# Optimization experiments

Measured on AMD Instinct MI355X. Metric: run time of the kernel, lower is better.

## Reference

```python
import jax, jax.numpy as jnp
import numpy as np

B, D, C = 4096, 256, 64  # batch, dim_embed, n_conditions
EPS = 1e-10


def setup_inputs() -> dict:
    key = jax.random.key(0)
    k1, k2, k3, k4 = jax.random.split(key, 4)
    x = jax.random.normal(k1, (B, D), dtype=jnp.float32)          # embedded_x (embeddingnet = identity)
    W = jax.random.normal(k2, (C, D, D), dtype=jnp.float32) * 0.02  # per-condition Linear weights (out,in)
    b = jax.random.normal(k3, (C, D), dtype=jnp.float32) * 0.02     # per-condition Linear biases
    c = jax.random.randint(k4, (B,), 0, C)                         # condition index per sample
    return {"x": x, "W": W, "b": b, "c": c}


def reference(x, W, b, c):
    # per-sample expert Linear: y_i = W[c_i] @ x_i + b[c_i]
    y = jnp.einsum('bij,bj->bi', W[c], x) + b[c]          # [B, D]
    # mask_norm accumulates L1 norm of the selected weight PER SAMPLE (duplicates counted)
    per_cond_l1 = jnp.sum(jnp.abs(W), axis=(1, 2))        # [C]
    mask_norm = jnp.sum(per_cond_l1[c])
    # embed_norm = global L2 (Frobenius) norm of embedded_x
    embed_norm = jnp.sqrt(jnp.sum(x * x))
    # F.normalize(p=2, dim=1, eps=1e-10): divide by max(row_norm, eps)
    row_norm = jnp.sqrt(jnp.sum(y * y, axis=1, keepdims=True))
    masked_embedding = y / jnp.maximum(row_norm, EPS)
    return (masked_embedding, mask_norm, embed_norm, x)
```

## Files before the change

kernel.cpp:

```cpp
#include <hip/hip_runtime.h>
#include <math.h>

#define B_ 4096
#define D_ 256
#define C_ 64
#define BD (B_*D_)

typedef __attribute__((ext_vector_type(8))) short bf16x8;
typedef __attribute__((ext_vector_type(4))) float f32x4;

__device__ __forceinline__ float wave_reduce_sum(float v) {
    #pragma unroll
    for (int off = 1; off < 64; off <<= 1) v += __shfl_xor(v, off);
    return v;
}

__device__ __forceinline__ float dpp_sum16(float v) {
    int t;
    t = __builtin_amdgcn_update_dpp(0, __float_as_int(v), 0x121, 0xF, 0xF, true); v += __int_as_float(t);
    t = __builtin_amdgcn_update_dpp(0, __float_as_int(v), 0x122, 0xF, 0xF, true); v += __int_as_float(t);
    t = __builtin_amdgcn_update_dpp(0, __float_as_int(v), 0x124, 0xF, 0xF, true); v += __int_as_float(t);
    t = __builtin_amdgcn_update_dpp(0, __float_as_int(v), 0x128, 0xF, 0xF, true); v += __int_as_float(t);
    return v;
}

__device__ __forceinline__ unsigned cvtpk(float lo, float hi) {
    unsigned r;
    asm volatile("v_cvt_pk_bf16_f32 %0, %1, %2" : "=v"(r) : "v"(lo), "v"(hi));
    return r;
}

__device__ __forceinline__ void cvt_store(const float4* wr, unsigned* dst, int do_l1, float& l1acc) {
    #pragma unroll
    for (int q = 0; q < 4; ++q) {
        uint4 pk;
        pk.x = cvtpk(wr[2*q].x,   wr[2*q].y);
        pk.y = cvtpk(wr[2*q].z,   wr[2*q].w);
        pk.z = cvtpk(wr[2*q+1].x, wr[2*q+1].y);
        pk.w = cvtpk(wr[2*q+1].z, wr[2*q+1].w);
        *(uint4*)(dst + q*4) = pk;
    }
    if (do_l1) {
        #pragma unroll
        for (int j = 0; j < 8; ++j)
            l1acc += fabsf(wr[j].x) + fabsf(wr[j].y) + fabsf(wr[j].z) + fabsf(wr[j].w);
    }
}

__global__ __launch_bounds__(256, 1) void k_main(const float* __restrict__ W,
                                                 const float* __restrict__ b,
                                                 const float* __restrict__ x,
                                                 const int* __restrict__ c,
                                                 float* __restrict__ out,
                                                 float* __restrict__ l1p,
                                                 float* __restrict__ xsqp,
                                                 int* __restrict__ cnt4) {
    int hw = blockIdx.x;
    int bid = (hw & 7) * 32 + (hw >> 3);
    int cond = bid >> 2;
    int sl = bid & 3;
    int tid = threadIdx.x;
    int wv = tid >> 6, lane = tid & 63;
    int g = lane >> 4, fr = lane & 15;

    const float4* x4 = (const float4*)x;
    float4 xv[4];
    #pragma unroll
    for (int t = 0; t < 4; ++t) xv[t] = x4[bid * 1024 + t * 256 + tid];
    int4 cvq[4];
    #pragma unroll
    for (int t = 0; t < 4; ++t) cvq[t] = ((const int4*)c)[t * 256 + tid];
    const float4* Wc4 = (const float4*)(W + (size_t)cond * 65536);
    float4 wrA[8], wrB[8];
    #pragma unroll
    for (int j = 0; j < 8; ++j) wrA[j] = Wc4[tid * 64 + j];
    float bias_v[4];
    #pragma unroll
    for (int nt = 0; nt < 4; ++nt) bias_v[nt] = b[cond * 256 + wv * 64 + nt * 16 + fr];

    __shared__ unsigned Xl[64 * 128];
    __shared__ unsigned Wl[2][256 * 20];
    __shared__ float wsums[4][64];
    __shared__ float part_x[4];
    __shared__ float part_w[4];
    __shared__ int slist[64];
    __shared__ int nlist;
    if (tid == 0) nlist = 0;

    float2* dst = (float2*)(out + BD + 2);
    float s = 0.f;
    #pragma unroll
    for (int t = 0; t < 4; ++t) {
        int xi = bid * 1024 + t * 256 + tid;
        dst[2 * xi]     = make_float2(xv[t].x, xv[t].y);
        dst[2 * xi + 1] = make_float2(xv[t].z, xv[t].w);
        s += xv[t].x * xv[t].x + xv[t].y * xv[t].y + xv[t].z * xv[t].z + xv[t].w * xv[t].w;
    }
    s = wave_reduce_sum(s);
    if (lane == 0) part_x[wv] = s;
    __syncthreads();

    #pragma unroll
    for (int t = 0; t < 4; ++t) {
        int4 q = cvq[t];
        int cc = (sl == 0) ? q.x : (sl == 1) ? q.y : (sl == 2) ? q.z : q.w;
        if (cc == cond) {
            int p = atomicAdd(&nlist, 1);
            if (p < 64) slist[p] = 4 * (t * 256 + tid) + sl;
        }
    }
    __syncthreads();
    int n = min(nlist, 64);
    int mts = (n + 15) >> 4;
    if (tid == 0) {
        xsqp[bid] = (part_x[0] + part_x[1]) + (part_x[2] + part_x[3]);
        cnt4[bid] = n;
    }

    for (int u = tid; u < n * 64; u += 256) {
        int si = u >> 6, v = u & 63;
        int sg = slist[si];
        float4 q = x4[(size_t)sg * 64 + v];
        int off = (v * 8) ^ ((si & 7) << 4);
        Xl[si * 128 + (off >> 2)]     = cvtpk(q.x, q.y);
        Xl[si * 128 + (off >> 2) + 1] = cvtpk(q.z, q.w);
    }

    float l1acc = 0.f;
    cvt_store(wrA, &Wl[0][tid * 20], sl == 0, l1acc);
    #pragma unroll
    for (int j = 0; j < 8; ++j) wrB[j] = Wc4[tid * 64 + 8 + j];
    __syncthreads();

    f32x4 acc[4][4];
    #pragma unroll
    for (int mt = 0; mt < 4; ++mt)
        #pragma unroll
        for (int nt = 0; nt < 4; ++nt)
            acc[mt][nt] = (f32x4){0.f, 0.f, 0.f, 0.f};

    #pragma unroll
    for (int kk = 0; kk < 8; ++kk) {
        const unsigned* Wb = Wl[kk & 1];
        bf16x8 bfr[4];
        #pragma unroll
        for (int nt = 0; nt < 4; ++nt)
            bfr[nt] = *(const bf16x8*)((const char*)Wb + ((wv * 64 + nt * 16 + fr) * 20 + g * 4) * 4);
        #pragma unroll
        for (int mt = 0; mt < 4; ++mt) if (mt < mts) {
            int row = mt * 16 + fr;
            bf16x8 afr = *(const bf16x8*)((const char*)Xl + row * 512 + ((kk * 64 + g * 16) ^ ((row & 7) << 4)));
            #pragma unroll
            for (int nt = 0; nt < 4; ++nt)
                acc[mt][nt] = __builtin_amdgcn_mfma_f32_16x16x32_bf16(afr, bfr[nt], acc[mt][nt], 0, 0, 0);
        }
        if (kk < 7) {
            if ((kk & 1) == 0) {
                cvt_store(wrB, &Wl[1][tid * 20], sl == 0, l1acc);
                if (kk < 6) {
                    #pragma unroll
                    for (int j = 0; j < 8; ++j) wrA[j] = Wc4[tid * 64 + (kk + 2) * 8 + j];
                }
            } else {
                cvt_store(wrA, &Wl[0][tid * 20], sl == 0, l1acc);
                if (kk < 6) {
                    #pragma unroll
                    for (int j = 0; j < 8; ++j) wrB[j] = Wc4[tid * 64 + (kk + 2) * 8 + j];
                }
            }
            __syncthreads();
        }
    }

    #pragma unroll
    for (int mt = 0; mt < 4; ++mt) if (mt < mts) {
        #pragma unroll
        for (int nt = 0; nt < 4; ++nt)
            #pragma unroll
            for (int j = 0; j < 4; ++j)
                acc[mt][nt][j] += bias_v[nt];
    }
    if (sl == 0) {
        float a = wave_reduce_sum(l1acc);
        if (lane == 0) part_w[wv] = a;
    }
    #pragma unroll
    for (int mt = 0; mt < 4; ++mt) if (mt < mts) {
        #pragma unroll
        for (int j = 0; j < 4; ++j) {
            float sj = acc[mt][0][j] * acc[mt][0][j] + acc[mt][1][j] * acc[mt][1][j]
                     + acc[mt][2][j] * acc[mt][2][j] + acc[mt][3][j] * acc[mt][3][j];
            sj = dpp_sum16(sj);
            if (fr == 0) wsums[wv][mt * 16 + g * 4 + j] = sj;
        }
    }
    __syncthreads();
    if (sl == 0 && tid == 0)
        l1p[cond] = (part_w[0] + part_w[1]) + (part_w[2] + part_w[3]);

    #pragma unroll
    for (int mt = 0; mt < 4; ++mt) if (mt < mts) {
        #pragma unroll
        for (int j = 0; j < 4; ++j) {
            int row = mt * 16 + g * 4 + j;
            if (row < n) {
                float tot = wsums[0][row] + wsums[1][row] + wsums[2][row] + wsums[3][row];
                float inv = 1.0f / fmaxf(sqrtf(tot), 1e-10f);
                int sgl = slist[row];
                float* op = out + (size_t)sgl * 256 + wv * 64 + fr;
                #pragma unroll
                for (int nt = 0; nt < 4; ++nt)
                    op[nt * 16] = acc[mt][nt][j] * inv;
            }
        }
    }
}

__global__ __launch_bounds__(256) void k_fin(const float* __restrict__ xsqp,
                                             const float* __restrict__ l1p,
                                             const int* __restrict__ cnt4,
                                             float* __restrict__ out) {
    int tid = threadIdx.x;
    int wv = tid >> 6, lane = tid & 63;
    __shared__ float part[4];
    float s = xsqp[tid];
    s = wave_reduce_sum(s);
    if (lane == 0) part[wv] = s;
    __syncthreads();
    if (tid == 0) out[BD + 1] = sqrtf((part[0] + part[1]) + (part[2] + part[3]));
    if (tid < 64) {
        float mv = l1p[tid] * (float)(cnt4[4 * tid] + cnt4[4 * tid + 1] + cnt4[4 * tid + 2] + cnt4[4 * tid + 3]);
        mv = wave_reduce_sum(mv);
        if (tid == 0) out[BD] = mv;
    }
}

extern "C" void kernel_launch(void* const* d_in, const int* in_sizes, int n_in,
                              void* d_out, int out_size, void* d_ws, size_t ws_size,
                              hipStream_t stream) {
    const float* x = (const float*)d_in[0];
    const float* W = (const float*)d_in[1];
    const float* b = (const float*)d_in[2];
    const int*   c = (const int*)d_in[3];
    float* out = (float*)d_out;

    float* xsqp = (float*)d_ws;
    float* l1p  = xsqp + 256;
    int*   cnt4 = (int*)(l1p + 64);

    k_main<<<256, 256, 0, stream>>>(W, b, x, c, out, l1p, xsqp, cnt4);
    k_fin<<<1, 256, 0, stream>>>(xsqp, l1p, cnt4, out);
}
```

Before: 20.96 us.

## Split work per condition by output column tile and move row normalization to second kernel

```diff
diff --git a/kernel.cpp b/kernel.cpp
--- a/kernel.cpp
+++ b/kernel.cpp
@@ -15,36 +15,10 @@
     return v;
 }
 
-__device__ __forceinline__ float dpp_sum16(float v) {
-    int t;
-    t = __builtin_amdgcn_update_dpp(0, __float_as_int(v), 0x121, 0xF, 0xF, true); v += __int_as_float(t);
-    t = __builtin_amdgcn_update_dpp(0, __float_as_int(v), 0x122, 0xF, 0xF, true); v += __int_as_float(t);
-    t = __builtin_amdgcn_update_dpp(0, __float_as_int(v), 0x124, 0xF, 0xF, true); v += __int_as_float(t);
-    t = __builtin_amdgcn_update_dpp(0, __float_as_int(v), 0x128, 0xF, 0xF, true); v += __int_as_float(t);
-    return v;
-}
-
 __device__ __forceinline__ unsigned cvtpk(float lo, float hi) {
     unsigned r;
     asm volatile("v_cvt_pk_bf16_f32 %0, %1, %2" : "=v"(r) : "v"(lo), "v"(hi));
     return r;
-}
-
-__device__ __forceinline__ void cvt_store(const float4* wr, unsigned* dst, int do_l1, float& l1acc) {
-    #pragma unroll
-    for (int q = 0; q < 4; ++q) {
-        uint4 pk;
-        pk.x = cvtpk(wr[2*q].x,   wr[2*q].y);
-        pk.y = cvtpk(wr[2*q].z,   wr[2*q].w);
-        pk.z = cvtpk(wr[2*q+1].x, wr[2*q+1].y);
-        pk.w = cvtpk(wr[2*q+1].z, wr[2*q+1].w);
-        *(uint4*)(dst + q*4) = pk;
-    }
-    if (do_l1) {
-        #pragma unroll
-        for (int j = 0; j < 8; ++j)
-            l1acc += fabsf(wr[j].x) + fabsf(wr[j].y) + fabsf(wr[j].z) + fabsf(wr[j].w);
-    }
 }
 
 __global__ __launch_bounds__(256, 1) void k_main(const float* __restrict__ W,
@@ -54,14 +28,15 @@
                                                  float* __restrict__ out,
                                                  float* __restrict__ l1p,
                                                  float* __restrict__ xsqp,
-                                                 int* __restrict__ cnt4) {
+                                                 int* __restrict__ cnt) {
     int hw = blockIdx.x;
     int bid = (hw & 7) * 32 + (hw >> 3);
     int cond = bid >> 2;
-    int sl = bid & 3;
+    int ct = bid & 3;
     int tid = threadIdx.x;
     int wv = tid >> 6, lane = tid & 63;
     int g = lane >> 4, fr = lane & 15;
+    int r = tid >> 2, ch = tid & 3;
 
     const float4* x4 = (const float4*)x;
     float4 xv[4];
@@ -70,20 +45,16 @@
     int4 cvq[4];
     #pragma unroll
     for (int t = 0; t < 4; ++t) cvq[t] = ((const int4*)c)[t * 256 + tid];
-    const float4* Wc4 = (const float4*)(W + (size_t)cond * 65536);
-    float4 wrA[8], wrB[8];
-    #pragma unroll
-    for (int j = 0; j < 8; ++j) wrA[j] = Wc4[tid * 64 + j];
-    float bias_v[4];
-    #pragma unroll
-    for (int nt = 0; nt < 4; ++nt) bias_v[nt] = b[cond * 256 + wv * 64 + nt * 16 + fr];
-
-    __shared__ unsigned Xl[64 * 128];
-    __shared__ unsigned Wl[2][256 * 20];
-    __shared__ float wsums[4][64];
+    const float4* Wr4 = (const float4*)(W + (size_t)cond * 65536 + (size_t)ct * 64 * 256) + (size_t)r * 64;
+    float4 wA0 = Wr4[ch * 2], wA1 = Wr4[ch * 2 + 1];
+    float4 wB0, wB1;
+    float bias_s = b[cond * 256 + ct * 64 + wv * 16 + fr];
+
+    __shared__ unsigned Xl[128 * 128];
+    __shared__ unsigned Wl[2][64 * 20];
     __shared__ float part_x[4];
     __shared__ float part_w[4];
-    __shared__ int slist[64];
+    __shared__ int slist[128];
     __shared__ int nlist;
     if (tid == 0) nlist = 0;
 
@@ -103,18 +74,18 @@
     #pragma unroll
     for (int t = 0; t < 4; ++t) {
         int4 q = cvq[t];
-        int cc = (sl == 0) ? q.x : (sl == 1) ? q.y : (sl == 2) ? q.z : q.w;
-        if (cc == cond) {
-            int p = atomicAdd(&nlist, 1);
-            if (p < 64) slist[p] = 4 * (t * 256 + tid) + sl;
-        }
-    }
-    __syncthreads();
-    int n = min(nlist, 64);
+        int base = 4 * (t * 256 + tid);
+        if (q.x == cond) { int p = atomicAdd(&nlist, 1); if (p < 128) slist[p] = base; }
+        if (q.y == cond) { int p = atomicAdd(&nlist, 1); if (p < 128) slist[p] = base + 1; }
+        if (q.z == cond) { int p = atomicAdd(&nlist, 1); if (p < 128) slist[p] = base + 2; }
+        if (q.w == cond) { int p = atomicAdd(&nlist, 1); if (p < 128) slist[p] = base + 3; }
+    }
+    __syncthreads();
+    int n = min(nlist, 128);
     int mts = (n + 15) >> 4;
     if (tid == 0) {
         xsqp[bid] = (part_x[0] + part_x[1]) + (part_x[2] + part_x[3]);
-        cnt4[bid] = n;
+        if (ct == 0) cnt[cond] = n;
     }
 
     for (int u = tid; u < n * 64; u += 256) {
@@ -127,112 +98,95 @@
     }
 
     float l1acc = 0.f;
-    cvt_store(wrA, &Wl[0][tid * 20], sl == 0, l1acc);
-    #pragma unroll
-    for (int j = 0; j < 8; ++j) wrB[j] = Wc4[tid * 64 + 8 + j];
-    __syncthreads();
-
-    f32x4 acc[4][4];
-    #pragma unroll
-    for (int mt = 0; mt < 4; ++mt)
-        #pragma unroll
-        for (int nt = 0; nt < 4; ++nt)
-            acc[mt][nt] = (f32x4){0.f, 0.f, 0.f, 0.f};
+    {
+        uint4 pk;
+        pk.x = cvtpk(wA0.x, wA0.y); pk.y = cvtpk(wA0.z, wA0.w);
+        pk.z = cvtpk(wA1.x, wA1.y); pk.w = cvtpk(wA1.z, wA1.w);
+        *(uint4*)(&Wl[0][r * 20 + ch * 4]) = pk;
+        l1acc += fabsf(wA0.x) + fabsf(wA0.y) + fabsf(wA0.z) + fabsf(wA0.w)
+               + fabsf(wA1.x) + fabsf(wA1.y) + fabsf(wA1.z) + fabsf(wA1.w);
+    }
+    wB0 = Wr4[8 + ch * 2]; wB1 = Wr4[8 + ch * 2 + 1];
+    __syncthreads();
+
+    f32x4 acc[8];
+    #pragma unroll
+    for (int mt = 0; mt < 8; ++mt) acc[mt] = (f32x4){0.f, 0.f, 0.f, 0.f};
 
     #pragma unroll
     for (int kk = 0; kk < 8; ++kk) {
         const unsigned* Wb = Wl[kk & 1];
-        bf16x8 bfr[4];
+        bf16x8 bfr = *(const bf16x8*)(Wb + (wv * 16 + fr) * 20 + g * 4);
         #pragma unroll
-        for (int nt = 0; nt < 4; ++nt)
-            bfr[nt] = *(const bf16x8*)((const char*)Wb + ((wv * 64 + nt * 16 + fr) * 20 + g * 4) * 4);
-        #pragma unroll
-        for (int mt = 0; mt < 4; ++mt) if (mt < mts) {
+        for (int mt = 0; mt < 8; ++mt) if (mt < mts) {
             int row = mt * 16 + fr;
             bf16x8 afr = *(const bf16x8*)((const char*)Xl + row * 512 + ((kk * 64 + g * 16) ^ ((row & 7) << 4)));
-            #pragma unroll
-            for (int nt = 0; nt < 4; ++nt)
-                acc[mt][nt] = __builtin_amdgcn_mfma_f32_16x16x32_bf16(afr, bfr[nt], acc[mt][nt], 0, 0, 0);
+            acc[mt] = __builtin_amdgcn_mfma_f32_16x16x32_bf16(afr, bfr, acc[mt], 0, 0, 0);
         }
         if (kk < 7) {
-            if ((kk & 1) == 0) {
-                cvt_store(wrB, &Wl[1][tid * 20], sl == 0, l1acc);
-                if (kk < 6) {
-                    #pragma unroll
-                    for (int j = 0; j < 8; ++j) wrA[j] = Wc4[tid * 64 + (kk + 2) * 8 + j];
-                }
-            } else {
-                cvt_store(wrA, &Wl[0][tid * 20], sl == 0, l1acc);
-                if (kk < 6) {
-                    #pragma unroll
-                    for (int j = 0; j < 8; ++j) wrB[j] = Wc4[tid * 64 + (kk + 2) * 8 + j];
-                }
+            float4 w0 = (kk & 1) ? wA0 : wB0;
+            float4 w1 = (kk & 1) ? wA1 : wB1;
+            uint4 pk;
+            pk.x = cvtpk(w0.x, w0.y); pk.y = cvtpk(w0.z, w0.w);
+            pk.z = cvtpk(w1.x, w1.y); pk.w = cvtpk(w1.z, w1.w);
+            *(uint4*)(&Wl[(kk + 1) & 1][r * 20 + ch * 4]) = pk;
+            l1acc += fabsf(w0.x) + fabsf(w0.y) + fabsf(w0.z) + fabsf(w0.w)
+                   + fabsf(w1.x) + fabsf(w1.y) + fabsf(w1.z) + fabsf(w1.w);
+            if (kk < 6) {
+                if (kk & 1) { wA0 = Wr4[(kk + 2) * 8 + ch * 2]; wA1 = Wr4[(kk + 2) * 8 + ch * 2 + 1]; }
+                else        { wB0 = Wr4[(kk + 2) * 8 + ch * 2]; wB1 = Wr4[(kk + 2) * 8 + ch * 2 + 1]; }
             }
             __syncthreads();
         }
     }
 
-    #pragma unroll
-    for (int mt = 0; mt < 4; ++mt) if (mt < mts) {
-        #pragma unroll
-        for (int nt = 0; nt < 4; ++nt)
-            #pragma unroll
-            for (int j = 0; j < 4; ++j)
-                acc[mt][nt][j] += bias_v[nt];
-    }
-    if (sl == 0) {
-        float a = wave_reduce_sum(l1acc);
-        if (lane == 0) part_w[wv] = a;
-    }
-    #pragma unroll
-    for (int mt = 0; mt < 4; ++mt) if (mt < mts) {
-        #pragma unroll
-        for (int j = 0; j < 4; ++j) {
-            float sj = acc[mt][0][j] * acc[mt][0][j] + acc[mt][1][j] * acc[mt][1][j]
-                     + acc[mt][2][j] * acc[mt][2][j] + acc[mt][3][j] * acc[mt][3][j];
-            sj = dpp_sum16(sj);
-            if (fr == 0) wsums[wv][mt * 16 + g * 4 + j] = sj;
-        }
-    }
-    __syncthreads();
-    if (sl == 0 && tid == 0)
-        l1p[cond] = (part_w[0] + part_w[1]) + (part_w[2] + part_w[3]);
-
-    #pragma unroll
-    for (int mt = 0; mt < 4; ++mt) if (mt < mts) {
+    float a = wave_reduce_sum(l1acc);
+    if (lane == 0) part_w[wv] = a;
+    __syncthreads();
+    if (tid == 0) l1p[bid] = (part_w[0] + part_w[1]) + (part_w[2] + part_w[3]);
+
+    #pragma unroll
+    for (int mt = 0; mt < 8; ++mt) if (mt < mts) {
         #pragma unroll
         for (int j = 0; j < 4; ++j) {
             int row = mt * 16 + g * 4 + j;
             if (row < n) {
-                float tot = wsums[0][row] + wsums[1][row] + wsums[2][row] + wsums[3][row];
-                float inv = 1.0f / fmaxf(sqrtf(tot), 1e-10f);
-                int sgl = slist[row];
-                float* op = out + (size_t)sgl * 256 + wv * 64 + fr;
-                #pragma unroll
-                for (int nt = 0; nt < 4; ++nt)
-                    op[nt * 16] = acc[mt][nt][j] * inv;
+                int sg = slist[row];
+                out[(size_t)sg * 256 + ct * 64 + wv * 16 + fr] = acc[mt][j] + bias_s;
             }
         }
     }
 }
 
-__global__ __launch_bounds__(256) void k_fin(const float* __restrict__ xsqp,
+__global__ __launch_bounds__(256) void k_fin(float* __restrict__ out,
+                                             const float* __restrict__ xsqp,
                                              const float* __restrict__ l1p,
-                                             const int* __restrict__ cnt4,
-                                             float* __restrict__ out) {
+                                             const int* __restrict__ cnt) {
     int tid = threadIdx.x;
     int wv = tid >> 6, lane = tid & 63;
-    __shared__ float part[4];
-    float s = xsqp[tid];
+    if (blockIdx.x == 1024) {
+        __shared__ float part[4];
+        float s = xsqp[tid];
+        s = wave_reduce_sum(s);
+        if (lane == 0) part[wv] = s;
+        __syncthreads();
+        if (tid < 64) {
+            float l1 = (l1p[tid * 4 + 0] + l1p[tid * 4 + 1]) + (l1p[tid * 4 + 2] + l1p[tid * 4 + 3]);
+            float mv = l1 * (float)cnt[tid];
+            mv = wave_reduce_sum(mv);
+            if (tid == 0) out[BD] = mv;
+        }
+        if (tid == 0) out[BD + 1] = sqrtf((part[0] + part[1]) + (part[2] + part[3]));
+        return;
+    }
+    int rowv = blockIdx.x * 4 + wv;
+    float4* p = (float4*)out + (size_t)rowv * 64 + lane;
+    float4 v = *p;
+    float s = v.x * v.x + v.y * v.y + v.z * v.z + v.w * v.w;
     s = wave_reduce_sum(s);
-    if (lane == 0) part[wv] = s;
-    __syncthreads();
-    if (tid == 0) out[BD + 1] = sqrtf((part[0] + part[1]) + (part[2] + part[3]));
-    if (tid < 64) {
-        float mv = l1p[tid] * (float)(cnt4[4 * tid] + cnt4[4 * tid + 1] + cnt4[4 * tid + 2] + cnt4[4 * tid + 3]);
-        mv = wave_reduce_sum(mv);
-        if (tid == 0) out[BD] = mv;
-    }
+    float inv = 1.0f / fmaxf(sqrtf(s), 1e-10f);
+    v.x *= inv; v.y *= inv; v.z *= inv; v.w *= inv;
+    *p = v;
 }
 
 extern "C" void kernel_launch(void* const* d_in, const int* in_sizes, int n_in,
@@ -246,8 +200,8 @@
 
     float* xsqp = (float*)d_ws;
     float* l1p  = xsqp + 256;
-    int*   cnt4 = (int*)(l1p + 64);
-
-    k_main<<<256, 256, 0, stream>>>(W, b, x, c, out, l1p, xsqp, cnt4);
-    k_fin<<<1, 256, 0, stream>>>(xsqp, l1p, cnt4, out);
-}
+    int*   cnt  = (int*)(l1p + 256);
+
+    k_main<<<256, 256, 0, stream>>>(W, b, x, c, out, l1p, xsqp, cnt);
+    k_fin<<<1025, 256, 0, stream>>>(out, xsqp, l1p, cnt);
+}
```

New measurement: 32.50 us. +55.0%, slower.
